# Performance work log

Measured on AMD Instinct MI355X. Metric: run time of the kernel, lower is better.

## Reference

```python
import jax, jax.numpy as jnp
import numpy as np

N = 50000      # nodes
E = 500000     # edges
MUL = 32       # multiplicity of 0e and 1o in node irreps
NUM_NEIGHBORS = 10.0
MIX = 0.15
INV3 = 1.0 / np.sqrt(3.0)  # sqrt(2*l3+1)*wigner_3j(1,1,0) = delta_ij/sqrt(3)


def setup_inputs() -> dict:
    key = jax.random.key(0)
    ks = jax.random.split(key, 16)
    f32 = jnp.float32
    node_input = jax.random.normal(ks[0], (N, 128), dtype=f32)  # 32x0e (32) + 32x1o (96)
    # edge_attr = spherical harmonics lmax=1, component normalization: Y0=1, |Y1|=sqrt(3)
    y1 = jax.random.normal(ks[1], (E, 3), dtype=f32)
    y1 = jnp.sqrt(3.0) * y1 / jnp.linalg.norm(y1, axis=1, keepdims=True)
    edge_attr = jnp.concatenate([jnp.ones((E, 1), f32), y1], axis=1)  # [E,4]
    edge_scalars = jax.random.uniform(ks[2], (E, 8), dtype=f32)       # radial embedding
    edge_src = jax.random.randint(ks[3], (E,), 0, N)
    edge_dst = jax.random.randint(ks[4], (E,), 0, N)
    rn = lambda k, s: jax.random.normal(k, s, dtype=f32)
    return {
        "node_input": node_input, "edge_attr": edge_attr, "edge_scalars": edge_scalars,
        "W1_s": rn(ks[5], (MUL, 2 * MUL)),  # first Linear, 0e block: 32 -> 64 (=feat 32 + self 32)
        "W1_v": rn(ks[6], (MUL, 2 * MUL)),  # first Linear, 1o block
        "M0": rn(ks[7], (8, 32)), "M1": rn(ks[8], (32, 32)),  # weight MLP (fc_neurons=[32,32])
        "Wtp0": rn(ks[9], (32, MUL)),   # path 0e x 0e -> 0e
        "Wtp1": rn(ks[10], (32, MUL)),  # path 0e x 1o -> 1o
        "Wtp2": rn(ks[11], (32, MUL)),  # path 1o x 0e -> 1o
        "Wtp3": rn(ks[12], (32, MUL)),  # path 1o x 1o -> 0e
        "W2_s": rn(ks[13], (2 * MUL, MUL)),  # final Linear, 0e: 64 -> 32
        "W2_v": rn(ks[14], (2 * MUL, MUL)),  # final Linear, 1o: 64 -> 32
        "edge_src": edge_src, "edge_dst": edge_dst,
    }


def _forward(node_input, edge_attr, edge_scalars, W1_s, W1_v, M0, M1,
             Wtp0, Wtp1, Wtp2, Wtp3, W2_s, W2_v, edge_src, edge_dst):
    n = node_input.shape[0]
    s = node_input[:, :MUL]                       # [N,32]  0e
    v = node_input[:, MUL:].reshape(n, MUL, 3)    # [N,32,3] 1o
    # Linear(node_input.irreps + irreps_out): per-irrep mixing, fan-in normalized
    s_all = (s @ W1_s) / jnp.sqrt(jnp.float32(MUL))                    # [N,64]
    v_all = jnp.einsum('nuk,uw->nwk', v, W1_v) / jnp.sqrt(jnp.float32(MUL))  # [N,64,3]
    feat_s, self_s = s_all[:, :MUL], s_all[:, MUL:]
    feat_v, self_v = v_all[:, :MUL], v_all[:, MUL:]

    # gather by edge source
    es = feat_s[edge_src]   # [E,32]
    ev = feat_v[edge_src]   # [E,32,3]
    y0 = edge_attr[:, 0]    # [E]
    y1 = edge_attr[:, 1:4]  # [E,3]

    # MLP on edge scalars -> per-edge, per-path 'uvu' weights (fan-in normalized)
    h = jax.nn.gelu(edge_scalars @ M0 / jnp.sqrt(jnp.float32(8)))
    h = jax.nn.gelu(h @ M1 / jnp.sqrt(jnp.float32(32)))                # [E,32]
    inv_sqrt_h = 1.0 / jnp.sqrt(jnp.float32(32))
    w0 = (h @ Wtp0) * inv_sqrt_h  # [E,32]
    w1 = (h @ Wtp1) * inv_sqrt_h
    w2 = (h @ Wtp2) * inv_sqrt_h
    w3 = (h @ Wtp3) * inv_sqrt_h

    # per-edge CG tensor product (4 'uvu' instructions)
    out0a = w0 * es * y0[:, None]                                    # 0e x 0e -> 0e
    out0b = w3 * jnp.einsum('euk,ek->eu', ev, y1) * INV3             # 1o x 1o -> 0e
    out1a = w1[:, :, None] * es[:, :, None] * y1[:, None, :]        # 0e x 1o -> 1o
    out1b = w2[:, :, None] * ev * y0[:, None, None]                 # 1o x 0e -> 1o
    out0 = jnp.concatenate([out0a, out0b], axis=1)                  # [E,64]  64x0e
    out1 = jnp.concatenate([out1a, out1b], axis=1)                  # [E,64,3] 64x1o

    # scatter-add to destination nodes, normalize by sqrt(num_neighbors)
    inv_deg = 1.0 / jnp.sqrt(jnp.float32(NUM_NEIGHBORS))
    ns = jax.ops.segment_sum(out0, edge_dst, num_segments=n) * inv_deg              # [N,64]
    nv = jax.ops.segment_sum(out1.reshape(-1, 2 * MUL * 3), edge_dst,
                             num_segments=n).reshape(n, 2 * MUL, 3) * inv_deg       # [N,64,3]

    # final per-irrep Linear to output irreps 32x0e + 32x1o
    conv_s = (ns @ W2_s) / jnp.sqrt(jnp.float32(2 * MUL))
    conv_v = jnp.einsum('nuk,uw->nwk', nv, W2_v) / jnp.sqrt(jnp.float32(2 * MUL))

    a = jnp.sqrt(jnp.float32(1.0 - MIX))
    b = jnp.sqrt(jnp.float32(MIX))
    out_s = a * self_s + b * conv_s                                  # [N,32]
    out_v = (a * self_v + b * conv_v).reshape(n, MUL * 3)            # [N,96]
    return jnp.concatenate([out_s, out_v], axis=1)                   # [N,128]


def reference(node_input, edge_attr, edge_scalars, W1_s, W1_v, M0, M1,
              Wtp0, Wtp1, Wtp2, Wtp3, W2_s, W2_v, edge_src, edge_dst):
    return _forward(node_input, edge_attr, edge_scalars, W1_s, W1_v, M0, M1,
                    Wtp0, Wtp1, Wtp2, Wtp3, W2_s, W2_v, edge_src, edge_dst)
```

## Files before the change

### kernel.cpp

```cpp
#include <hip/hip_runtime.h>
#include <math.h>

#define N_NODES 50000
#define N_EDGES 500000
#define NPB 16
#define GROUPS 8

__device__ __forceinline__ float gelu_fast(float x) {
    const float k0 = 0.7978845608028654f;
    const float k1 = 0.044715f;
    float z2 = 2.f * k0 * (x + k1 * x * x * x);
    float ez = __expf(z2);
    float th = 1.f - 2.f * __builtin_amdgcn_rcpf(ez + 1.f);
    return 0.5f * x * (1.f + th);
}

__device__ __forceinline__ unsigned short f2bf(float x) {
    unsigned int u = __float_as_uint(x);
    unsigned int r = (u + 0x7FFFu + ((u >> 16) & 1u)) >> 16;
    return (unsigned short)r;
}
__device__ __forceinline__ unsigned int pack2bf(float a, float b) {
    return (unsigned int)f2bf(a) | ((unsigned int)f2bf(b) << 16);
}
__device__ __forceinline__ float bf2f(unsigned short b) {
    return __uint_as_float(((unsigned int)b) << 16);
}

__device__ __forceinline__ void lds_add(float* p, float v) {
    unsigned int off = (unsigned int)(size_t)p;
    asm volatile("ds_add_f32 %0, %1" :: "v"(off), "v"(v) : "memory");
}

__global__ void node_pre(const float* __restrict__ node_input,
                         const float* __restrict__ W1_s,
                         const float* __restrict__ W1_v,
                         float* __restrict__ feat,
                         float* __restrict__ out) {
    __shared__ float lWs[32 * 64];
    __shared__ float lWv[32 * 64];
    for (int i = threadIdx.x; i < 2048; i += blockDim.x) {
        lWs[i] = W1_s[i];
        lWv[i] = W1_v[i];
    }
    __syncthreads();
    int n = blockIdx.x * blockDim.x + threadIdx.x;
    if (n >= N_NODES) return;
    const float inv_sqrt_mul = 0.17677669529663687f;
    const float a_mix = 0.9219544457292887f;

    float s[32];
#pragma unroll
    for (int u = 0; u < 32; ++u) s[u] = node_input[n * 128 + u];
#pragma unroll 4
    for (int w = 0; w < 64; ++w) {
        float acc = 0.f;
#pragma unroll
        for (int u = 0; u < 32; ++u) acc += s[u] * lWs[u * 64 + w];
        acc *= inv_sqrt_mul;
        if (w < 32) feat[(size_t)n * 128 + w * 4 + 0] = acc;
        else        out[n * 128 + (w - 32)] = a_mix * acc;
    }
#pragma unroll
    for (int k = 0; k < 3; ++k) {
        float vk[32];
#pragma unroll
        for (int u = 0; u < 32; ++u) vk[u] = node_input[n * 128 + 32 + u * 3 + k];
#pragma unroll 4
        for (int w = 0; w < 64; ++w) {
            float acc = 0.f;
#pragma unroll
            for (int u = 0; u < 32; ++u) acc += vk[u] * lWv[u * 64 + w];
            acc *= inv_sqrt_mul;
            if (w < 32) feat[(size_t)n * 128 + w * 4 + 1 + k] = acc;
            else        out[n * 128 + 32 + (w - 32) * 3 + k] = a_mix * acc;
        }
    }
}

__global__ void hist_kernel(const int* __restrict__ edge_dst, int* __restrict__ counts) {
    int e = blockIdx.x * blockDim.x + threadIdx.x;
    if (e < N_EDGES) atomicAdd(&counts[edge_dst[e]], 1);
}

__global__ void scan_kernel(const int* __restrict__ counts,
                            int* __restrict__ offsets,
                            int* __restrict__ cursor) {
    const int T = 1024;
    __shared__ int partial[T];
    int t = threadIdx.x;
    const int chunk = (N_NODES + T - 1) / T;
    int start = t * chunk;
    int end = start + chunk; if (end > N_NODES) end = N_NODES;
    if (start > N_NODES) start = N_NODES;
    int sum = 0;
    for (int i = start; i < end; ++i) sum += counts[i];
    partial[t] = sum;
    __syncthreads();
    for (int off = 1; off < T; off <<= 1) {
        int other = (t >= off) ? partial[t - off] : 0;
        __syncthreads();
        partial[t] += other;
        __syncthreads();
    }
    int run = (t == 0) ? 0 : partial[t - 1];
    for (int i = start; i < end; ++i) {
        offsets[i] = run;
        cursor[i] = run;
        run += counts[i];
    }
    if (t == T - 1) offsets[N_NODES] = run;
}

__global__ void scatter_kernel(const int* __restrict__ edge_src,
                               const int* __restrict__ edge_dst,
                               const float* __restrict__ edge_attr,
                               int* __restrict__ cursor,
                               float4* __restrict__ ySorted,
                               int4* __restrict__ sde) {
    int e = blockIdx.x * blockDim.x + threadIdx.x;
    if (e >= N_EDGES) return;
    int d = edge_dst[e];
    int pos = atomicAdd(&cursor[d], 1);
    ySorted[pos] = *(const float4*)(edge_attr + (size_t)e * 4);
    sde[pos] = make_int4(edge_src[e], d, e, 0);
}

__global__ void __launch_bounds__(256)
mlp_kernel(const float* __restrict__ edge_scalars,
           const float* __restrict__ M0,
           const float* __restrict__ M1,
           const float* __restrict__ Wtp0,
           const float* __restrict__ Wtp1,
           const float* __restrict__ Wtp2,
           const float* __restrict__ Wtp3,
           uint4* __restrict__ wOut16) {
    __shared__ uint4 stage[4][328];

    const int wv   = threadIdx.x >> 6;
    const int lane = threadIdx.x & 63;
    const int e0w  = blockIdx.x * 256 + wv * 64;
    int e = e0w + lane;
    int ec = e < N_EDGES ? e : N_EDGES - 1;

    const float inv_sqrt8  = 0.35355339059327373f;
    const float inv_sqrt32 = 0.17677669529663687f;

    const float4 s0 = *(const float4*)(edge_scalars + (size_t)ec * 8);
    const float4 s1 = *(const float4*)(edge_scalars + (size_t)ec * 8 + 4);

    float t[32];
#pragma unroll
    for (int u = 0; u < 32; ++u) {
        float acc = s0.x * M0[0 * 32 + u] + s0.y * M0[1 * 32 + u]
                  + s0.z * M0[2 * 32 + u] + s0.w * M0[3 * 32 + u]
                  + s1.x * M0[4 * 32 + u] + s1.y * M0[5 * 32 + u]
                  + s1.z * M0[6 * 32 + u] + s1.w * M0[7 * 32 + u];
        t[u] = gelu_fast(acc * inv_sqrt8);
    }
    float h[32];
#pragma unroll
    for (int u = 0; u < 32; ++u) {
        float acc = 0.f;
#pragma unroll
        for (int m = 0; m < 32; ++m) acc += t[m] * M1[m * 32 + u];
        h[u] = gelu_fast(acc * inv_sqrt32);
    }

#pragma unroll 1
    for (int q = 0; q < 4; ++q) {
#pragma unroll
        for (int col = 0; col < 4; ++col) {
            const int u = q * 8 + col * 2;
            float a0 = 0.f, b0 = 0.f, c0 = 0.f, d0 = 0.f;
            float a1 = 0.f, b1 = 0.f, c1 = 0.f, d1 = 0.f;
#pragma unroll
            for (int j = 0; j < 32; ++j) {
                const float hj = h[j];
                a0 += hj * Wtp0[j * 32 + u];
                b0 += hj * Wtp1[j * 32 + u];
                c0 += hj * Wtp2[j * 32 + u];
                d0 += hj * Wtp3[j * 32 + u];
                a1 += hj * Wtp0[j * 32 + u + 1];
                b1 += hj * Wtp1[j * 32 + u + 1];
                c1 += hj * Wtp2[j * 32 + u + 1];
                d1 += hj * Wtp3[j * 32 + u + 1];
            }
            uint4 pk;
            pk.x = pack2bf(a0 * inv_sqrt32, b0 * inv_sqrt32);
            pk.y = pack2bf(c0 * inv_sqrt32, d0 * inv_sqrt32);
            pk.z = pack2bf(a1 * inv_sqrt32, b1 * inv_sqrt32);
            pk.w = pack2bf(c1 * inv_sqrt32, d1 * inv_sqrt32);
            stage[wv][lane * 5 + (lane >> 3) + col] = pk;
        }
        asm volatile("s_waitcnt lgkmcnt(0)" ::: "memory");
#pragma unroll
        for (int p = 0; p < 4; ++p) {
            const int el  = p * 16 + (lane >> 2);
            const int col = lane & 3;
            const uint4 v = stage[wv][el * 5 + (el >> 3) + col];
            const int ge = e0w + el;
            if (ge < N_EDGES)
                wOut16[(size_t)ge * 16 + q * 4 + col] = v;
        }
        asm volatile("s_waitcnt lgkmcnt(0)" ::: "memory");
    }
}

__global__ void __launch_bounds__(256)
conv_kernel(const ushort4* __restrict__ wOut,
            const float4* __restrict__ ySorted,
            const int4* __restrict__ sde,
            const int* __restrict__ offsets,
            const float* __restrict__ W2_s,
            const float* __restrict__ W2_v,
            const float* __restrict__ feat,
            float* __restrict__ out) {
    __shared__ float sacc[NPB * 256];
    for (int i = threadIdx.x; i < NPB * 256; i += blockDim.x) sacc[i] = 0.f;
    __syncthreads();

    const int lane = threadIdx.x & 31;
    const int g = threadIdx.x >> 5;
    const int n0 = blockIdx.x * NPB;
    const int eb = offsets[n0];
    const int ee = offsets[n0 + NPB];
    const float INV3 = 0.5773502691896258f;
    const float4* feat4 = (const float4*)feat;

    const int total = ee - eb;
    const int per = (total + GROUPS - 1) / GROUPS;
    const int es = eb + g * per;
    int et = es + per; if (et > ee) et = ee;

    float r0 = 0.f, r1 = 0.f, r2 = 0.f, r3 = 0.f;
    float r4 = 0.f, r5 = 0.f, r6 = 0.f, r7 = 0.f;
    int cur = -1;

#pragma unroll 2
    for (int e = es; e < et; ++e) {
        const int4 sd = sde[e];
        const ushort4 wq = wOut[(size_t)sd.z * 32 + lane];
        const float4 yq = ySorted[e];
        const float4 f = feat4[(size_t)sd.x * 32 + lane];

        if (sd.y != cur) {
            if (cur >= 0) {
                float* a = sacc + (cur - n0) * 256;
                lds_add(a + lane, r0);
                lds_add(a + 32 + lane, r1);
                lds_add(a + 64 + lane * 3 + 0, r2);
                lds_add(a + 64 + lane * 3 + 1, r3);
                lds_add(a + 64 + lane * 3 + 2, r4);
                lds_add(a + 160 + lane * 3 + 0, r5);
                lds_add(a + 160 + lane * 3 + 1, r6);
                lds_add(a + 160 + lane * 3 + 2, r7);
            }
            cur = sd.y;
            r0 = r1 = r2 = r3 = r4 = r5 = r6 = r7 = 0.f;
        }

        const float w0 = bf2f(wq.x), w1 = bf2f(wq.y);
        const float w2 = bf2f(wq.z), w3 = bf2f(wq.w);
        const float dvy = f.y * yq.y + f.z * yq.z + f.w * yq.w;
        const float w1es = w1 * f.x;
        const float w2y0 = w2 * yq.x;

        r0 += w0 * f.x * yq.x;
        r1 += w3 * dvy * INV3;
        r2 += w1es * yq.y;
        r3 += w1es * yq.z;
        r4 += w1es * yq.w;
        r5 += w2y0 * f.y;
        r6 += w2y0 * f.z;
        r7 += w2y0 * f.w;
    }
    if (cur >= 0) {
        float* a = sacc + (cur - n0) * 256;
        lds_add(a + lane, r0);
        lds_add(a + 32 + lane, r1);
        lds_add(a + 64 + lane * 3 + 0, r2);
        lds_add(a + 64 + lane * 3 + 1, r3);
        lds_add(a + 64 + lane * 3 + 2, r4);
        lds_add(a + 160 + lane * 3 + 0, r5);
        lds_add(a + 160 + lane * 3 + 1, r6);
        lds_add(a + 160 + lane * 3 + 2, r7);
    }
    asm volatile("s_waitcnt lgkmcnt(0)" ::: "memory");
    __syncthreads();

    const float scale = 0.31622776601683794f * 0.125f * 0.3872983346207417f;
    for (int li = g; li < NPB; li += GROUPS) {
        const float* a = sacc + li * 256;
        float cs = 0.f, cv0 = 0.f, cv1 = 0.f, cv2 = 0.f;
#pragma unroll 8
        for (int j = 0; j < 64; ++j) {
            const float as = a[j];
            cs += as * __ldg(&W2_s[j * 32 + lane]);
            const float wv = __ldg(&W2_v[j * 32 + lane]);
            cv0 += a[64 + 3 * j + 0] * wv;
            cv1 += a[64 + 3 * j + 1] * wv;
            cv2 += a[64 + 3 * j + 2] * wv;
        }
        float* o = out + (size_t)(n0 + li) * 128;
        o[lane]              += scale * cs;
        o[32 + lane * 3 + 0] += scale * cv0;
        o[32 + lane * 3 + 1] += scale * cv1;
        o[32 + lane * 3 + 2] += scale * cv2;
    }
}

extern "C" void kernel_launch(void* const* d_in, const int* in_sizes, int n_in,
                              void* d_out, int out_size, void* d_ws, size_t ws_size,
                              hipStream_t stream) {
    const float* node_input   = (const float*)d_in[0];
    const float* edge_attr    = (const float*)d_in[1];
    const float* edge_scalars = (const float*)d_in[2];
    const float* W1_s = (const float*)d_in[3];
    const float* W1_v = (const float*)d_in[4];
    const float* M0   = (const float*)d_in[5];
    const float* M1   = (const float*)d_in[6];
    const float* Wtp0 = (const float*)d_in[7];
    const float* Wtp1 = (const float*)d_in[8];
    const float* Wtp2 = (const float*)d_in[9];
    const float* Wtp3 = (const float*)d_in[10];
    const float* W2_s = (const float*)d_in[11];
    const float* W2_v = (const float*)d_in[12];
    const int* edge_src = (const int*)d_in[13];
    const int* edge_dst = (const int*)d_in[14];
    float* out = (float*)d_out;
    float* ws  = (float*)d_ws;

    float*  feat    = ws;
    float4* ySorted = (float4*)(feat + (size_t)N_NODES * 128);
    ushort4* wOut   = (ushort4*)(ySorted + N_EDGES);
    int4*  sde      = (int4*)(wOut + (size_t)N_EDGES * 32);
    int*   counts   = (int*)(sde + N_EDGES);
    int*   offsets  = counts + N_NODES;
    int*   cursor   = offsets + N_NODES + 1;

    hipMemsetAsync(counts, 0, N_NODES * sizeof(int), stream);

    node_pre<<<(N_NODES + 255) / 256, 256, 0, stream>>>(node_input, W1_s, W1_v,
                                                        feat, out);

    hist_kernel<<<(N_EDGES + 255) / 256, 256, 0, stream>>>(edge_dst, counts);
    scan_kernel<<<1, 1024, 0, stream>>>(counts, offsets, cursor);
    scatter_kernel<<<(N_EDGES + 255) / 256, 256, 0, stream>>>(edge_src, edge_dst,
                                                              edge_attr,
                                                              cursor, ySorted, sde);

    mlp_kernel<<<(N_EDGES + 255) / 256, 256, 0, stream>>>(edge_scalars, M0, M1,
                                                          Wtp0, Wtp1, Wtp2, Wtp3,
                                                          (uint4*)wOut);

    conv_kernel<<<N_NODES / NPB, 256, 0, stream>>>(wOut, ySorted, sde, offsets,
                                                   W2_s, W2_v, feat, out);
}
```

Before: 577.8 us.

## Compute per-edge weight MLP with bf16 MFMA in a persistent grid

Rewrites the edge weight MLP (8->32->32->4x32) to use 32x32x16 bf16 matrix-core instructions instead of per-thread scalar FMAs. Weight fragments are preloaded once per wave, and waves loop persistently over 32-edge tiles on a fixed 512-block grid. Activations are repacked between layers with cross-half shuffles, and outputs are staged through LDS for coalesced stores. The hidden activations are now rounded to bf16, which adds rounding error in exchange for much higher arithmetic throughput on the MLP.

```diff
diff --git a/kernel.cpp b/kernel.cpp
--- a/kernel.cpp
+++ b/kernel.cpp
@@ -5,6 +5,9 @@
 #define N_EDGES 500000
 #define NPB 16
 #define GROUPS 8
+
+typedef __attribute__((ext_vector_type(8))) short bf16x8;
+typedef __attribute__((ext_vector_type(16))) float f32x16;
 
 __device__ __forceinline__ float gelu_fast(float x) {
     const float k0 = 0.7978845608028654f;
@@ -30,6 +33,13 @@
 __device__ __forceinline__ void lds_add(float* p, float v) {
     unsigned int off = (unsigned int)(size_t)p;
     asm volatile("ds_add_f32 %0, %1" :: "v"(off), "v"(v) : "memory");
+}
+
+__device__ __forceinline__ bf16x8 mk_frag4(unsigned int w0, unsigned int w1,
+                                           unsigned int w2, unsigned int w3) {
+    union { unsigned int u[4]; bf16x8 v; } x;
+    x.u[0] = w0; x.u[1] = w1; x.u[2] = w2; x.u[3] = w3;
+    return x.v;
 }
 
 __global__ void node_pre(const float* __restrict__ node_input,
@@ -135,73 +145,146 @@
            const float* __restrict__ Wtp2,
            const float* __restrict__ Wtp3,
            uint4* __restrict__ wOut16) {
-    __shared__ uint4 stage[4][328];
+    __shared__ unsigned int smem[4 * 68 * 32];
 
     const int wv   = threadIdx.x >> 6;
     const int lane = threadIdx.x & 63;
-    const int e0w  = blockIdx.x * 256 + wv * 64;
-    int e = e0w + lane;
-    int ec = e < N_EDGES ? e : N_EDGES - 1;
+    const int col  = lane & 31;
+    const int a    = lane >> 5;
+    unsigned int* wsm = smem + wv * (68 * 32);
 
     const float inv_sqrt8  = 0.35355339059327373f;
     const float inv_sqrt32 = 0.17677669529663687f;
 
-    const float4 s0 = *(const float4*)(edge_scalars + (size_t)ec * 8);
-    const float4 s1 = *(const float4*)(edge_scalars + (size_t)ec * 8 + 4);
-
-    float t[32];
-#pragma unroll
-    for (int u = 0; u < 32; ++u) {
-        float acc = s0.x * M0[0 * 32 + u] + s0.y * M0[1 * 32 + u]
-                  + s0.z * M0[2 * 32 + u] + s0.w * M0[3 * 32 + u]
-                  + s1.x * M0[4 * 32 + u] + s1.y * M0[5 * 32 + u]
-                  + s1.z * M0[6 * 32 + u] + s1.w * M0[7 * 32 + u];
-        t[u] = gelu_fast(acc * inv_sqrt8);
-    }
-    float h[32];
-#pragma unroll
-    for (int u = 0; u < 32; ++u) {
-        float acc = 0.f;
-#pragma unroll
-        for (int m = 0; m < 32; ++m) acc += t[m] * M1[m * 32 + u];
-        h[u] = gelu_fast(acc * inv_sqrt32);
-    }
+    bf16x8 A1, A2[2], A3[4][2];
+    {
+        union { short h[8]; bf16x8 v; } x;
+#pragma unroll
+        for (int i = 0; i < 8; ++i)
+            x.h[i] = (a == 0) ? (short)f2bf(M0[i * 32 + col]) : (short)0;
+        A1 = x.v;
+#pragma unroll
+        for (int ks = 0; ks < 2; ++ks) {
+            union { short h[8]; bf16x8 v; } y;
+#pragma unroll
+            for (int i = 0; i < 8; ++i)
+                y.h[i] = (short)f2bf(M1[(ks * 16 + a * 8 + i) * 32 + col]);
+            A2[ks] = y.v;
+        }
+        const float* Wsel = (lane & 3) == 0 ? Wtp0 :
+                            (lane & 3) == 1 ? Wtp1 :
+                            (lane & 3) == 2 ? Wtp2 : Wtp3;
+        const int colw0 = (col >> 2);
+#pragma unroll
+        for (int t = 0; t < 4; ++t) {
+#pragma unroll
+            for (int ks = 0; ks < 2; ++ks) {
+                union { short h[8]; bf16x8 v; } y;
+#pragma unroll
+                for (int i = 0; i < 8; ++i)
+                    y.h[i] = (short)f2bf(Wsel[(ks * 16 + a * 8 + i) * 32 + t * 8 + colw0]);
+                A3[t][ks] = y.v;
+            }
+        }
+    }
+
+    const int wave_id = blockIdx.x * 4 + wv;
+    const int n_waves = gridDim.x * 4;
+    const int NB = N_EDGES / 32;
+
+    for (int b = wave_id; b < NB; b += n_waves) {
+        const int e0 = b * 32;
+
+        bf16x8 B1;
+        {
+            union { short h[8]; bf16x8 v; } x;
+            if (a == 0) {
+                const float4 s0 = *(const float4*)(edge_scalars + (size_t)(e0 + col) * 8);
+                const float4 s1 = *(const float4*)(edge_scalars + (size_t)(e0 + col) * 8 + 4);
+                x.h[0] = (short)f2bf(s0.x); x.h[1] = (short)f2bf(s0.y);
+                x.h[2] = (short)f2bf(s0.z); x.h[3] = (short)f2bf(s0.w);
+                x.h[4] = (short)f2bf(s1.x); x.h[5] = (short)f2bf(s1.y);
+                x.h[6] = (short)f2bf(s1.z); x.h[7] = (short)f2bf(s1.w);
+            } else {
+#pragma unroll
+                for (int i = 0; i < 8; ++i) x.h[i] = 0;
+            }
+            B1 = x.v;
+        }
+
+        f32x16 d1;
+#pragma unroll
+        for (int r = 0; r < 16; ++r) d1[r] = 0.f;
+        d1 = __builtin_amdgcn_mfma_f32_32x32x16_bf16(A1, B1, d1, 0, 0, 0);
+
+        float g1[16];
+#pragma unroll
+        for (int r = 0; r < 16; ++r) g1[r] = gelu_fast(d1[r] * inv_sqrt8);
+
+        bf16x8 B2[2];
+        {
+            unsigned int p01 = pack2bf(g1[0], g1[1]),   p23 = pack2bf(g1[2], g1[3]);
+            unsigned int p45 = pack2bf(g1[4], g1[5]),   p67 = pack2bf(g1[6], g1[7]);
+            unsigned int p89 = pack2bf(g1[8], g1[9]),   pAB = pack2bf(g1[10], g1[11]);
+            unsigned int pCD = pack2bf(g1[12], g1[13]), pEF = pack2bf(g1[14], g1[15]);
+            unsigned int q01 = __shfl_xor(p01, 32, 64), q23 = __shfl_xor(p23, 32, 64);
+            unsigned int q45 = __shfl_xor(p45, 32, 64), q67 = __shfl_xor(p67, 32, 64);
+            unsigned int q89 = __shfl_xor(p89, 32, 64), qAB = __shfl_xor(pAB, 32, 64);
+            unsigned int qCD = __shfl_xor(pCD, 32, 64), qEF = __shfl_xor(pEF, 32, 64);
+            B2[0] = a ? mk_frag4(q45, q67, p45, p67) : mk_frag4(p01, p23, q01, q23);
+            B2[1] = a ? mk_frag4(qCD, qEF, pCD, pEF) : mk_frag4(p89, pAB, q89, qAB);
+        }
+
+        f32x16 d2;
+#pragma unroll
+        for (int r = 0; r < 16; ++r) d2[r] = 0.f;
+        d2 = __builtin_amdgcn_mfma_f32_32x32x16_bf16(A2[0], B2[0], d2, 0, 0, 0);
+        d2 = __builtin_amdgcn_mfma_f32_32x32x16_bf16(A2[1], B2[1], d2, 0, 0, 0);
+
+        float g2[16];
+#pragma unroll
+        for (int r = 0; r < 16; ++r) g2[r] = gelu_fast(d2[r] * inv_sqrt32);
+
+        bf16x8 B3[2];
+        {
+            unsigned int p01 = pack2bf(g2[0], g2[1]),   p23 = pack2bf(g2[2], g2[3]);
+            unsigned int p45 = pack2bf(g2[4], g2[5]),   p67 = pack2bf(g2[6], g2[7]);
+            unsigned int p89 = pack2bf(g2[8], g2[9]),   pAB = pack2bf(g2[10], g2[11]);
+            unsigned int pCD = pack2bf(g2[12], g2[13]), pEF = pack2bf(g2[14], g2[15]);
+            unsigned int q01 = __shfl_xor(p01, 32, 64), q23 = __shfl_xor(p23, 32, 64);
+            unsigned int q45 = __shfl_xor(p45, 32, 64), q67 = __shfl_xor(p67, 32, 64);
+            unsigned int q89 = __shfl_xor(p89, 32, 64), qAB = __shfl_xor(pAB, 32, 64);
+            unsigned int qCD = __shfl_xor(pCD, 32, 64), qEF = __shfl_xor(pEF, 32, 64);
+            B3[0] = a ? mk_frag4(q45, q67, p45, p67) : mk_frag4(p01, p23, q01, q23);
+            B3[1] = a ? mk_frag4(qCD, qEF, pCD, pEF) : mk_frag4(p89, pAB, q89, qAB);
+        }
 
 #pragma unroll 1
-    for (int q = 0; q < 4; ++q) {
-#pragma unroll
-        for (int col = 0; col < 4; ++col) {
-            const int u = q * 8 + col * 2;
-            float a0 = 0.f, b0 = 0.f, c0 = 0.f, d0 = 0.f;
-            float a1 = 0.f, b1 = 0.f, c1 = 0.f, d1 = 0.f;
-#pragma unroll
-            for (int j = 0; j < 32; ++j) {
-                const float hj = h[j];
-                a0 += hj * Wtp0[j * 32 + u];
-                b0 += hj * Wtp1[j * 32 + u];
-                c0 += hj * Wtp2[j * 32 + u];
-                d0 += hj * Wtp3[j * 32 + u];
-                a1 += hj * Wtp0[j * 32 + u + 1];
-                b1 += hj * Wtp1[j * 32 + u + 1];
-                c1 += hj * Wtp2[j * 32 + u + 1];
-                d1 += hj * Wtp3[j * 32 + u + 1];
+        for (int t = 0; t < 4; ++t) {
+            f32x16 d3;
+#pragma unroll
+            for (int r = 0; r < 16; ++r) d3[r] = 0.f;
+            d3 = __builtin_amdgcn_mfma_f32_32x32x16_bf16(A3[t][0], B3[0], d3, 0, 0, 0);
+            d3 = __builtin_amdgcn_mfma_f32_32x32x16_bf16(A3[t][1], B3[1], d3, 0, 0, 0);
+#pragma unroll
+            for (int q = 0; q < 4; ++q) {
+                unsigned int w0 = pack2bf(d3[4 * q + 0] * inv_sqrt32,
+                                          d3[4 * q + 1] * inv_sqrt32);
+                unsigned int w1 = pack2bf(d3[4 * q + 2] * inv_sqrt32,
+                                          d3[4 * q + 3] * inv_sqrt32);
+                const int dw = col * 68 + (t * 16 + 4 * q + 2 * a);
+                uint2 pk; pk.x = w0; pk.y = w1;
+                *(uint2*)&wsm[dw] = pk;
             }
-            uint4 pk;
-            pk.x = pack2bf(a0 * inv_sqrt32, b0 * inv_sqrt32);
-            pk.y = pack2bf(c0 * inv_sqrt32, d0 * inv_sqrt32);
-            pk.z = pack2bf(a1 * inv_sqrt32, b1 * inv_sqrt32);
-            pk.w = pack2bf(c1 * inv_sqrt32, d1 * inv_sqrt32);
-            stage[wv][lane * 5 + (lane >> 3) + col] = pk;
         }
         asm volatile("s_waitcnt lgkmcnt(0)" ::: "memory");
-#pragma unroll
-        for (int p = 0; p < 4; ++p) {
-            const int el  = p * 16 + (lane >> 2);
-            const int col = lane & 3;
-            const uint4 v = stage[wv][el * 5 + (el >> 3) + col];
-            const int ge = e0w + el;
-            if (ge < N_EDGES)
-                wOut16[(size_t)ge * 16 + q * 4 + col] = v;
+
+#pragma unroll
+        for (int it = 0; it < 8; ++it) {
+            const int e = it * 4 + (lane >> 4);
+            const int c = lane & 15;
+            const uint4 v = *(const uint4*)&wsm[e * 68 + c * 4];
+            wOut16[(size_t)(e0 + e) * 16 + c] = v;
         }
         asm volatile("s_waitcnt lgkmcnt(0)" ::: "memory");
     }
@@ -246,15 +329,15 @@
 
         if (sd.y != cur) {
             if (cur >= 0) {
-                float* a = sacc + (cur - n0) * 256;
-                lds_add(a + lane, r0);
-                lds_add(a + 32 + lane, r1);
-                lds_add(a + 64 + lane * 3 + 0, r2);
-                lds_add(a + 64 + lane * 3 + 1, r3);
-                lds_add(a + 64 + lane * 3 + 2, r4);
-                lds_add(a + 160 + lane * 3 + 0, r5);
-                lds_add(a + 160 + lane * 3 + 1, r6);
-                lds_add(a + 160 + lane * 3 + 2, r7);
+                float* ap = sacc + (cur - n0) * 256;
+                lds_add(ap + lane, r0);
+                lds_add(ap + 32 + lane, r1);
+                lds_add(ap + 64 + lane * 3 + 0, r2);
+                lds_add(ap + 64 + lane * 3 + 1, r3);
+                lds_add(ap + 64 + lane * 3 + 2, r4);
+                lds_add(ap + 160 + lane * 3 + 0, r5);
+                lds_add(ap + 160 + lane * 3 + 1, r6);
+                lds_add(ap + 160 + lane * 3 + 2, r7);
             }
             cur = sd.y;
             r0 = r1 = r2 = r3 = r4 = r5 = r6 = r7 = 0.f;
@@ -276,31 +359,31 @@
         r7 += w2y0 * f.w;
     }
     if (cur >= 0) {
-        float* a = sacc + (cur - n0) * 256;
-        lds_add(a + lane, r0);
-        lds_add(a + 32 + lane, r1);
-        lds_add(a + 64 + lane * 3 + 0, r2);
-        lds_add(a + 64 + lane * 3 + 1, r3);
-        lds_add(a + 64 + lane * 3 + 2, r4);
-        lds_add(a + 160 + lane * 3 + 0, r5);
-        lds_add(a + 160 + lane * 3 + 1, r6);
-        lds_add(a + 160 + lane * 3 + 2, r7);
+        float* ap = sacc + (cur - n0) * 256;
+        lds_add(ap + lane, r0);
+        lds_add(ap + 32 + lane, r1);
+        lds_add(ap + 64 + lane * 3 + 0, r2);
+        lds_add(ap + 64 + lane * 3 + 1, r3);
+        lds_add(ap + 64 + lane * 3 + 2, r4);
+        lds_add(ap + 160 + lane * 3 + 0, r5);
+        lds_add(ap + 160 + lane * 3 + 1, r6);
+        lds_add(ap + 160 + lane * 3 + 2, r7);
     }
     asm volatile("s_waitcnt lgkmcnt(0)" ::: "memory");
     __syncthreads();
 
     const float scale = 0.31622776601683794f * 0.125f * 0.3872983346207417f;
     for (int li = g; li < NPB; li += GROUPS) {
-        const float* a = sacc + li * 256;
+        const float* ap = sacc + li * 256;
         float cs = 0.f, cv0 = 0.f, cv1 = 0.f, cv2 = 0.f;
 #pragma unroll 8
         for (int j = 0; j < 64; ++j) {
-            const float as = a[j];
+            const float as = ap[j];
             cs += as * __ldg(&W2_s[j * 32 + lane]);
             const float wv = __ldg(&W2_v[j * 32 + lane]);
-            cv0 += a[64 + 3 * j + 0] * wv;
-            cv1 += a[64 + 3 * j + 1] * wv;
-            cv2 += a[64 + 3 * j + 2] * wv;
+            cv0 += ap[64 + 3 * j + 0] * wv;
+            cv1 += ap[64 + 3 * j + 1] * wv;
+            cv2 += ap[64 + 3 * j + 2] * wv;
         }
         float* o = out + (size_t)(n0 + li) * 128;
         o[lane]              += scale * cs;
@@ -350,9 +433,9 @@
                                                               edge_attr,
                                                               cursor, ySorted, sde);
 
-    mlp_kernel<<<(N_EDGES + 255) / 256, 256, 0, stream>>>(edge_scalars, M0, M1,
-                                                          Wtp0, Wtp1, Wtp2, Wtp3,
-                                                          (uint4*)wOut);
+    mlp_kernel<<<512, 256, 0, stream>>>(edge_scalars, M0, M1,
+                                        Wtp0, Wtp1, Wtp2, Wtp3,
+                                        (uint4*)wOut);
 
     conv_kernel<<<N_NODES / NPB, 256, 0, stream>>>(wOut, ySorted, sde, offsets,
                                                    W2_s, W2_v, feat, out);
```

Result: slower. 667.4 us (+15.5%).

## Store hidden MLP activations and fuse final weight projection into conv kernel

Applied to the files above, without the earlier changes.

The edge MLP kernel no longer computes and writes the 128 per-edge tensor-product weights. It now writes only the 32-wide hidden activation h in bf16, cutting per-edge intermediate storage from 256 to 64 bytes. The conv kernel keeps the Wtp matrices per lane in registers as packed bf16 and recomputes the four path weights per edge with 64 extra FMAs. This trades DRAM traffic for extra ALU work and register pressure in the gather loop, and the Wtp weights are now rounded to bf16 as well.

```diff
diff --git a/kernel.cpp b/kernel.cpp
--- a/kernel.cpp
+++ b/kernel.cpp
@@ -23,8 +23,11 @@
 __device__ __forceinline__ unsigned int pack2bf(float a, float b) {
     return (unsigned int)f2bf(a) | ((unsigned int)f2bf(b) << 16);
 }
-__device__ __forceinline__ float bf2f(unsigned short b) {
-    return __uint_as_float(((unsigned int)b) << 16);
+__device__ __forceinline__ float bf_lo(unsigned int w) {
+    return __uint_as_float(w << 16);
+}
+__device__ __forceinline__ float bf_hi(unsigned int w) {
+    return __uint_as_float(w & 0xffff0000u);
 }
 
 __device__ __forceinline__ void lds_add(float* p, float v) {
@@ -127,15 +130,11 @@
 }
 
 __global__ void __launch_bounds__(256)
-mlp_kernel(const float* __restrict__ edge_scalars,
-           const float* __restrict__ M0,
-           const float* __restrict__ M1,
-           const float* __restrict__ Wtp0,
-           const float* __restrict__ Wtp1,
-           const float* __restrict__ Wtp2,
-           const float* __restrict__ Wtp3,
-           uint4* __restrict__ wOut16) {
-    __shared__ uint4 stage[4][328];
+h_kernel(const float* __restrict__ edge_scalars,
+         const float* __restrict__ M0,
+         const float* __restrict__ M1,
+         uint4* __restrict__ hOut) {
+    __shared__ unsigned int stage[256 * 20];
 
     const int wv   = threadIdx.x >> 6;
     const int lane = threadIdx.x & 63;
@@ -167,61 +166,58 @@
         h[u] = gelu_fast(acc * inv_sqrt32);
     }
 
-#pragma unroll 1
-    for (int q = 0; q < 4; ++q) {
-#pragma unroll
-        for (int col = 0; col < 4; ++col) {
-            const int u = q * 8 + col * 2;
-            float a0 = 0.f, b0 = 0.f, c0 = 0.f, d0 = 0.f;
-            float a1 = 0.f, b1 = 0.f, c1 = 0.f, d1 = 0.f;
-#pragma unroll
-            for (int j = 0; j < 32; ++j) {
-                const float hj = h[j];
-                a0 += hj * Wtp0[j * 32 + u];
-                b0 += hj * Wtp1[j * 32 + u];
-                c0 += hj * Wtp2[j * 32 + u];
-                d0 += hj * Wtp3[j * 32 + u];
-                a1 += hj * Wtp0[j * 32 + u + 1];
-                b1 += hj * Wtp1[j * 32 + u + 1];
-                c1 += hj * Wtp2[j * 32 + u + 1];
-                d1 += hj * Wtp3[j * 32 + u + 1];
-            }
-            uint4 pk;
-            pk.x = pack2bf(a0 * inv_sqrt32, b0 * inv_sqrt32);
-            pk.y = pack2bf(c0 * inv_sqrt32, d0 * inv_sqrt32);
-            pk.z = pack2bf(a1 * inv_sqrt32, b1 * inv_sqrt32);
-            pk.w = pack2bf(c1 * inv_sqrt32, d1 * inv_sqrt32);
-            stage[wv][lane * 5 + (lane >> 3) + col] = pk;
-        }
-        asm volatile("s_waitcnt lgkmcnt(0)" ::: "memory");
-#pragma unroll
-        for (int p = 0; p < 4; ++p) {
-            const int el  = p * 16 + (lane >> 2);
-            const int col = lane & 3;
-            const uint4 v = stage[wv][el * 5 + (el >> 3) + col];
-            const int ge = e0w + el;
-            if (ge < N_EDGES)
-                wOut16[(size_t)ge * 16 + q * 4 + col] = v;
-        }
-        asm volatile("s_waitcnt lgkmcnt(0)" ::: "memory");
+    unsigned int* myrow = stage + threadIdx.x * 20;
+#pragma unroll
+    for (int c = 0; c < 4; ++c) {
+        uint4 pk;
+        pk.x = pack2bf(h[c * 8 + 0], h[c * 8 + 1]);
+        pk.y = pack2bf(h[c * 8 + 2], h[c * 8 + 3]);
+        pk.z = pack2bf(h[c * 8 + 4], h[c * 8 + 5]);
+        pk.w = pack2bf(h[c * 8 + 6], h[c * 8 + 7]);
+        *(uint4*)&myrow[c * 4] = pk;
+    }
+    asm volatile("s_waitcnt lgkmcnt(0)" ::: "memory");
+#pragma unroll
+    for (int p = 0; p < 4; ++p) {
+        const int el = p * 16 + (lane >> 2);
+        const int c  = lane & 3;
+        const uint4 v = *(const uint4*)&stage[(wv * 64 + el) * 20 + c * 4];
+        const int ge = e0w + el;
+        if (ge < N_EDGES)
+            hOut[(size_t)ge * 4 + c] = v;
     }
 }
 
 __global__ void __launch_bounds__(256)
-conv_kernel(const ushort4* __restrict__ wOut,
+conv_kernel(const uint4* __restrict__ hBuf,
             const float4* __restrict__ ySorted,
             const int4* __restrict__ sde,
             const int* __restrict__ offsets,
+            const float* __restrict__ Wtp0,
+            const float* __restrict__ Wtp1,
+            const float* __restrict__ Wtp2,
+            const float* __restrict__ Wtp3,
             const float* __restrict__ W2_s,
             const float* __restrict__ W2_v,
             const float* __restrict__ feat,
             float* __restrict__ out) {
     __shared__ float sacc[NPB * 256];
     for (int i = threadIdx.x; i < NPB * 256; i += blockDim.x) sacc[i] = 0.f;
-    __syncthreads();
 
     const int lane = threadIdx.x & 31;
     const int g = threadIdx.x >> 5;
+
+    const float inv_sqrt32 = 0.17677669529663687f;
+    unsigned int wA[32], wB[32];
+#pragma unroll
+    for (int j = 0; j < 32; ++j) {
+        wA[j] = pack2bf(Wtp0[j * 32 + lane] * inv_sqrt32,
+                        Wtp1[j * 32 + lane] * inv_sqrt32);
+        wB[j] = pack2bf(Wtp2[j * 32 + lane] * inv_sqrt32,
+                        Wtp3[j * 32 + lane] * inv_sqrt32);
+    }
+    __syncthreads();
+
     const int n0 = blockIdx.x * NPB;
     const int eb = offsets[n0];
     const int ee = offsets[n0 + NPB];
@@ -237,31 +233,48 @@
     float r4 = 0.f, r5 = 0.f, r6 = 0.f, r7 = 0.f;
     int cur = -1;
 
-#pragma unroll 2
     for (int e = es; e < et; ++e) {
         const int4 sd = sde[e];
-        const ushort4 wq = wOut[(size_t)sd.z * 32 + lane];
         const float4 yq = ySorted[e];
         const float4 f = feat4[(size_t)sd.x * 32 + lane];
+        const uint4 hq0 = hBuf[(size_t)sd.z * 4 + 0];
+        const uint4 hq1 = hBuf[(size_t)sd.z * 4 + 1];
+        const uint4 hq2 = hBuf[(size_t)sd.z * 4 + 2];
+        const uint4 hq3 = hBuf[(size_t)sd.z * 4 + 3];
 
         if (sd.y != cur) {
             if (cur >= 0) {
-                float* a = sacc + (cur - n0) * 256;
-                lds_add(a + lane, r0);
-                lds_add(a + 32 + lane, r1);
-                lds_add(a + 64 + lane * 3 + 0, r2);
-                lds_add(a + 64 + lane * 3 + 1, r3);
-                lds_add(a + 64 + lane * 3 + 2, r4);
-                lds_add(a + 160 + lane * 3 + 0, r5);
-                lds_add(a + 160 + lane * 3 + 1, r6);
-                lds_add(a + 160 + lane * 3 + 2, r7);
+                float* ap = sacc + (cur - n0) * 256;
+                lds_add(ap + lane, r0);
+                lds_add(ap + 32 + lane, r1);
+                lds_add(ap + 64 + lane * 3 + 0, r2);
+                lds_add(ap + 64 + lane * 3 + 1, r3);
+                lds_add(ap + 64 + lane * 3 + 2, r4);
+                lds_add(ap + 160 + lane * 3 + 0, r5);
+                lds_add(ap + 160 + lane * 3 + 1, r6);
+                lds_add(ap + 160 + lane * 3 + 2, r7);
             }
             cur = sd.y;
             r0 = r1 = r2 = r3 = r4 = r5 = r6 = r7 = 0.f;
         }
 
-        const float w0 = bf2f(wq.x), w1 = bf2f(wq.y);
-        const float w2 = bf2f(wq.z), w3 = bf2f(wq.w);
+        float w0 = 0.f, w1 = 0.f, w2 = 0.f, w3 = 0.f;
+        unsigned int hw[16] = {hq0.x, hq0.y, hq0.z, hq0.w,
+                               hq1.x, hq1.y, hq1.z, hq1.w,
+                               hq2.x, hq2.y, hq2.z, hq2.w,
+                               hq3.x, hq3.y, hq3.z, hq3.w};
+#pragma unroll
+        for (int k = 0; k < 16; ++k) {
+            const float hlo = bf_lo(hw[k]);
+            const float hhi = bf_hi(hw[k]);
+            const unsigned int a0 = wA[2 * k],     b0 = wB[2 * k];
+            const unsigned int a1 = wA[2 * k + 1], b1 = wB[2 * k + 1];
+            w0 += hlo * bf_lo(a0); w1 += hlo * bf_hi(a0);
+            w2 += hlo * bf_lo(b0); w3 += hlo * bf_hi(b0);
+            w0 += hhi * bf_lo(a1); w1 += hhi * bf_hi(a1);
+            w2 += hhi * bf_lo(b1); w3 += hhi * bf_hi(b1);
+        }
+
         const float dvy = f.y * yq.y + f.z * yq.z + f.w * yq.w;
         const float w1es = w1 * f.x;
         const float w2y0 = w2 * yq.x;
@@ -276,31 +289,31 @@
         r7 += w2y0 * f.w;
     }
     if (cur >= 0) {
-        float* a = sacc + (cur - n0) * 256;
-        lds_add(a + lane, r0);
-        lds_add(a + 32 + lane, r1);
-        lds_add(a + 64 + lane * 3 + 0, r2);
-        lds_add(a + 64 + lane * 3 + 1, r3);
-        lds_add(a + 64 + lane * 3 + 2, r4);
-        lds_add(a + 160 + lane * 3 + 0, r5);
-        lds_add(a + 160 + lane * 3 + 1, r6);
-        lds_add(a + 160 + lane * 3 + 2, r7);
+        float* ap = sacc + (cur - n0) * 256;
+        lds_add(ap + lane, r0);
+        lds_add(ap + 32 + lane, r1);
+        lds_add(ap + 64 + lane * 3 + 0, r2);
+        lds_add(ap + 64 + lane * 3 + 1, r3);
+        lds_add(ap + 64 + lane * 3 + 2, r4);
+        lds_add(ap + 160 + lane * 3 + 0, r5);
+        lds_add(ap + 160 + lane * 3 + 1, r6);
+        lds_add(ap + 160 + lane * 3 + 2, r7);
     }
     asm volatile("s_waitcnt lgkmcnt(0)" ::: "memory");
     __syncthreads();
 
     const float scale = 0.31622776601683794f * 0.125f * 0.3872983346207417f;
     for (int li = g; li < NPB; li += GROUPS) {
-        const float* a = sacc + li * 256;
+        const float* ap = sacc + li * 256;
         float cs = 0.f, cv0 = 0.f, cv1 = 0.f, cv2 = 0.f;
 #pragma unroll 8
         for (int j = 0; j < 64; ++j) {
-            const float as = a[j];
+            const float as = ap[j];
             cs += as * __ldg(&W2_s[j * 32 + lane]);
             const float wv = __ldg(&W2_v[j * 32 + lane]);
-            cv0 += a[64 + 3 * j + 0] * wv;
-            cv1 += a[64 + 3 * j + 1] * wv;
-            cv2 += a[64 + 3 * j + 2] * wv;
+            cv0 += ap[64 + 3 * j + 0] * wv;
+            cv1 += ap[64 + 3 * j + 1] * wv;
+            cv2 += ap[64 + 3 * j + 2] * wv;
         }
         float* o = out + (size_t)(n0 + li) * 128;
         o[lane]              += scale * cs;
@@ -333,11 +346,11 @@
 
     float*  feat    = ws;
     float4* ySorted = (float4*)(feat + (size_t)N_NODES * 128);
-    ushort4* wOut   = (ushort4*)(ySorted + N_EDGES);
-    int4*  sde      = (int4*)(wOut + (size_t)N_EDGES * 32);
-    int*   counts   = (int*)(sde + N_EDGES);
-    int*   offsets  = counts + N_NODES;
-    int*   cursor   = offsets + N_NODES + 1;
+    uint4*  hBuf    = (uint4*)(ySorted + N_EDGES);
+    int4*   sde     = (int4*)(hBuf + (size_t)N_EDGES * 4);
+    int*    counts  = (int*)(sde + N_EDGES);
+    int*    offsets = counts + N_NODES;
+    int*    cursor  = offsets + N_NODES + 1;
 
     hipMemsetAsync(counts, 0, N_NODES * sizeof(int), stream);
 
@@ -350,10 +363,9 @@
                                                               edge_attr,
                                                               cursor, ySorted, sde);
 
-    mlp_kernel<<<(N_EDGES + 255) / 256, 256, 0, stream>>>(edge_scalars, M0, M1,
-                                                          Wtp0, Wtp1, Wtp2, Wtp3,
-                                                          (uint4*)wOut);
-
-    conv_kernel<<<N_NODES / NPB, 256, 0, stream>>>(wOut, ySorted, sde, offsets,
+    h_kernel<<<(N_EDGES + 255) / 256, 256, 0, stream>>>(edge_scalars, M0, M1, hBuf);
+
+    conv_kernel<<<N_NODES / NPB, 256, 0, stream>>>(hBuf, ySorted, sde, offsets,
+                                                   Wtp0, Wtp1, Wtp2, Wtp3,
                                                    W2_s, W2_v, feat, out);
 }
```

New measurement: 561.9 us. 1.03x faster.
